# Kernel tuning notes

Hardware: AMD Instinct MI355X
Metric: run time of the kernel (lower is better)

Reference implementation:

```python
import jax, jax.numpy as jnp
import numpy as np

B, C, R = 1024, 256, 7          # batch, channels, ROI feature map res
PATCH, DIL = 16, 2              # correlation patch size, dilation_patch
REP = 1024                      # representation_size
FLAT = PATCH * PATCH * R * R    # 12544 = fc1 input dim


def setup_inputs() -> dict:
    key = jax.random.key(0)
    k = jax.random.split(key, 8)
    return {
        "patch1": jax.random.normal(k[0], (B, C, R, R), dtype=jnp.float32),
        "patch2": jax.random.normal(k[1], (B, C, R, R), dtype=jnp.float32),
        "W1": jax.random.normal(k[2], (REP, FLAT), dtype=jnp.float32) * 0.01,
        "b1": jnp.zeros((REP,), dtype=jnp.float32),
        "W2": jax.random.normal(k[3], (REP, REP), dtype=jnp.float32) * 0.02,
        "b2": jnp.zeros((REP,), dtype=jnp.float32),
        "W3": jax.random.normal(k[4], (4, REP), dtype=jnp.float32) * 0.02,
        "b3": jnp.zeros((4,), dtype=jnp.float32),
    }


def _correlate(p1, p2):
    """SpatialCorrelationSampler(patch_size=16, dilation_patch=2), kernel=1, stride=1.
    out[b, pi, pj, i, j] = sum_c p1[b,c,i,j] * p2[b,c, i+(pi-8)*2, j+(pj-8)*2]
    (zero outside bounds). Returns [B, PATCH*PATCH, R, R]."""
    pad = (PATCH // 2) * DIL  # 16; displacements span [-16, 14]
    p2p = jnp.pad(p2, ((0, 0), (0, 0), (pad, pad), (pad, pad)))  # [B,C,39,39]
    outs = []
    for pi in range(PATCH):
        for pj in range(PATCH):
            # shifted window: row offset (pi-8)*2 + pad = 2*pi, same for cols
            win = p2p[:, :, DIL * pi:DIL * pi + R, DIL * pj:DIL * pj + R]
            outs.append(jnp.einsum('bchw,bchw->bhw', p1, win))
    return jnp.stack(outs, axis=1)  # [B, 256, 7, 7] -> matches torch flatten order


def reference(patch1, patch2, W1, b1, W2, b2, W3, b3):
    x = _correlate(patch1, patch2).reshape(patch1.shape[0], -1)  # [B, 12544]
    x = jax.nn.relu(x @ W1.T + b1)
    x = jax.nn.relu(x @ W2.T + b2)
    pred_boxes = x @ W3.T + b3  # [B, 4]
    return pred_boxes
```

## Files before the change

kernel.cpp:

```cpp
#include <hip/hip_runtime.h>

#define BATCH 1024
#define RR    49
#define SP    12544
#define KVALID 625
#define KPAD   640
#define REP_N  1024

typedef __attribute__((ext_vector_type(4))) float f32x4;
typedef __attribute__((ext_vector_type(8))) short s16x8;

__device__ __forceinline__ unsigned short f2bf_rne(float f) {
    unsigned int u = __float_as_uint(f);
    unsigned int r = u + 0x7FFFu + ((u >> 16) & 1u);
    return (unsigned short)(r >> 16);
}
__device__ __forceinline__ float bf2f(unsigned short h) {
    return __uint_as_float(((unsigned int)h) << 16);
}
__device__ __forceinline__ void split2(float v, unsigned short& h, unsigned short& l) {
    h = f2bf_rne(v);
    l = f2bf_rne(v - bf2f(h));
}

__device__ __forceinline__ void dec25(int u, int& i, int& d) {
    int ii = (u >= 4) + (u >= 7) + (u >= 11) + (u >= 14) + (u >= 18) + (u >= 21);
    int cum = (7 * ii + 1) >> 1;
    i = ii;
    d = 2 * (u - cum) + (ii & 1);
}
__device__ __forceinline__ int enc25(int i, int d) {
    return ((7 * i + 1) >> 1) + ((d - (i & 1)) >> 1);
}

__device__ __forceinline__ int kflat_of(int a) {
    int ar = a / 25, ac = a % 25;
    int i, dy, j, dx;
    dec25(ar, i, dy);
    dec25(ac, j, dx);
    int pi = (dy + 16 - i) >> 1;
    int pj = (dx + 16 - j) >> 1;
    return (pi * 16 + pj) * 49 + i * 7 + j;
}

#define MM(d, a, b) d = __builtin_amdgcn_mfma_f32_16x16x32_bf16(a, b, d, 0, 0, 0)

__global__ __launch_bounds__(256) void corr_gram_kernel(
    const float* __restrict__ p1, const float* __restrict__ p2,
    unsigned short* __restrict__ xh, unsigned short* __restrict__ xl)
{
    __shared__ unsigned short Ah[64][72];
    __shared__ unsigned short Al[64][72];
    __shared__ unsigned short Bh[64][72];
    __shared__ unsigned short Bl[64][72];

    const int b = blockIdx.x;
    const int t = threadIdx.x;
    const float* P1 = p1 + (size_t)b * SP;
    const float* P2 = p2 + (size_t)b * SP;

    const int wv   = t >> 6;
    const int lane = t & 63;
    const int wr = (wv >> 1) * 32;
    const int wc = (wv & 1) * 32;
    const int fr = lane & 15;
    const int fg = (lane >> 4) * 8;

    f32x4 acc00 = {}, acc01 = {}, acc10 = {}, acc11 = {};

    for (int cc = 0; cc < 4; ++cc) {
        __syncthreads();
        for (int j = t; j < 784; j += 256) {
            const int isB = (j >= 392);
            const int jj = isB ? j - 392 : j;
            const float* P = isB ? P2 : P1;
            unsigned short* Hp = isB ? &Bh[0][0] : &Ah[0][0];
            unsigned short* Lp = isB ? &Bl[0][0] : &Al[0][0];
            const int cg = jj / 49;
            const int s  = jj - cg * 49;
            const float* src = P + (cc * 64 + cg * 8) * 49 + s;
            float v[8];
            #pragma unroll
            for (int i = 0; i < 8; ++i) v[i] = src[i * 49];
            s16x8 hv, lv;
            #pragma unroll
            for (int i = 0; i < 8; ++i) {
                unsigned short h, l;
                split2(v[i], h, l);
                hv[i] = (short)h; lv[i] = (short)l;
            }
            *(s16x8*)&Hp[s * 72 + cg * 8] = hv;
            *(s16x8*)&Lp[s * 72 + cg * 8] = lv;
        }
        __syncthreads();

        #pragma unroll
        for (int ks = 0; ks < 2; ++ks) {
            const int ko = ks * 32 + fg;
            s16x8 ah0 = *(const s16x8*)&Ah[wr + fr][ko];
            s16x8 ah1 = *(const s16x8*)&Ah[wr + 16 + fr][ko];
            s16x8 al0 = *(const s16x8*)&Al[wr + fr][ko];
            s16x8 al1 = *(const s16x8*)&Al[wr + 16 + fr][ko];
            s16x8 bh0 = *(const s16x8*)&Bh[wc + fr][ko];
            s16x8 bh1 = *(const s16x8*)&Bh[wc + 16 + fr][ko];
            s16x8 bl0 = *(const s16x8*)&Bl[wc + fr][ko];
            s16x8 bl1 = *(const s16x8*)&Bl[wc + 16 + fr][ko];

            MM(acc00, ah0, bh0); MM(acc00, ah0, bl0); MM(acc00, al0, bh0);
            MM(acc01, ah0, bh1); MM(acc01, ah0, bl1); MM(acc01, al0, bh1);
            MM(acc10, ah1, bh0); MM(acc10, ah1, bl0); MM(acc10, al1, bh0);
            MM(acc11, ah1, bh1); MM(acc11, ah1, bl1); MM(acc11, al1, bh1);
        }
    }

    if (t < KPAD - KVALID) {
        xh[(size_t)b * KPAD + KVALID + t] = 0;
        xl[(size_t)b * KPAD + KVALID + t] = 0;
    }

    unsigned short* rh = xh + (size_t)b * KPAD;
    unsigned short* rl = xl + (size_t)b * KPAD;
    const int arow = (lane >> 4) * 4;
    #pragma unroll
    for (int nf = 0; nf < 2; ++nf) {
        const int n = wc + nf * 16 + fr;
        #pragma unroll
        for (int mf = 0; mf < 2; ++mf) {
            const f32x4 a = (nf == 0) ? (mf == 0 ? acc00 : acc10)
                                      : (mf == 0 ? acc01 : acc11);
            #pragma unroll
            for (int r = 0; r < 4; ++r) {
                const int m = wr + mf * 16 + arow + r;
                if (m < RR && n < RR) {
                    const int i  = m / 7, jj = m - i * 7;
                    const int dy = n / 7, dx = n - dy * 7;
                    if ((((i + dy) | (jj + dx)) & 1) == 0) {
                        const int aidx = enc25(i, dy) * 25 + enc25(jj, dx);
                        unsigned short h, l;
                        split2(a[r], h, l);
                        rh[aidx] = h; rl[aidx] = l;
                    }
                }
            }
        }
    }
}

__global__ __launch_bounds__(256) void prep_w1_kernel(
    const float* __restrict__ W1,
    unsigned short* __restrict__ wh, unsigned short* __restrict__ wl)
{
    int idx = blockIdx.x * 256 + threadIdx.x;
    int n = idx / KPAD, a = idx - n * KPAD;
    float v = 0.f;
    if (a < KVALID) v = W1[(size_t)n * SP + kflat_of(a)];
    unsigned short h, l;
    split2(v, h, l);
    wh[idx] = h; wl[idx] = l;
}

__global__ __launch_bounds__(256) void prep_w2_kernel(
    const float* __restrict__ W2,
    unsigned short* __restrict__ wh, unsigned short* __restrict__ wl)
{
    int idx = (blockIdx.x * 256 + threadIdx.x) * 4;
    float4 v = *(const float4*)&W2[idx];
    unsigned short h0, l0, h1, l1, h2, l2, h3, l3;
    split2(v.x, h0, l0); split2(v.y, h1, l1);
    split2(v.z, h2, l2); split2(v.w, h3, l3);
    ushort4 hv = make_ushort4(h0, h1, h2, h3);
    ushort4 lv = make_ushort4(l0, l1, l2, l3);
    *(ushort4*)&wh[idx] = hv;
    *(ushort4*)&wl[idx] = lv;
}

template<bool SPLIT_OUT>
__global__ __launch_bounds__(256) void gemm_mfma(
    const unsigned short* __restrict__ Xh, const unsigned short* __restrict__ Xl, int ldx,
    const unsigned short* __restrict__ Wh, const unsigned short* __restrict__ Wl, int ldw,
    const float* __restrict__ bias, int K,
    float* __restrict__ Yf, unsigned short* __restrict__ Yh, unsigned short* __restrict__ Yl,
    int ldy)
{
    __shared__ unsigned short As[2][64][72];
    __shared__ unsigned short Bs[2][64][72];

    const int t = threadIdx.x;
    const int m_base = blockIdx.y * 64;
    const int n_base = blockIdx.x * 64;

    const int trow = t >> 2;
    const int tc   = (t & 3) * 8;

    const unsigned short* xh_p = Xh + (size_t)(m_base + trow) * ldx + tc;
    const unsigned short* xl_p = Xl + (size_t)(m_base + trow) * ldx + tc;
    const unsigned short* wh_p = Wh + (size_t)(n_base + trow) * ldw + tc;
    const unsigned short* wl_p = Wl + (size_t)(n_base + trow) * ldw + tc;

    const int wv   = t >> 6;
    const int lane = t & 63;
    const int wr = (wv >> 1) * 32;
    const int wc = (wv & 1) * 32;
    const int fr = lane & 15;
    const int fg = (lane >> 4) * 8;

    f32x4 acc00 = {}, acc01 = {}, acc10 = {}, acc11 = {};

    for (int k0 = 0; k0 < K; k0 += 64) {
        s16x8 vxh0 = *(const s16x8*)(xh_p + k0);
        s16x8 vxh1 = *(const s16x8*)(xh_p + k0 + 32);
        s16x8 vxl0 = *(const s16x8*)(xl_p + k0);
        s16x8 vxl1 = *(const s16x8*)(xl_p + k0 + 32);
        s16x8 vwh0 = *(const s16x8*)(wh_p + k0);
        s16x8 vwh1 = *(const s16x8*)(wh_p + k0 + 32);
        s16x8 vwl0 = *(const s16x8*)(wl_p + k0);
        s16x8 vwl1 = *(const s16x8*)(wl_p + k0 + 32);
        __syncthreads();
        *(s16x8*)&As[0][trow][tc]      = vxh0;
        *(s16x8*)&As[0][trow][tc + 32] = vxh1;
        *(s16x8*)&As[1][trow][tc]      = vxl0;
        *(s16x8*)&As[1][trow][tc + 32] = vxl1;
        *(s16x8*)&Bs[0][trow][tc]      = vwh0;
        *(s16x8*)&Bs[0][trow][tc + 32] = vwh1;
        *(s16x8*)&Bs[1][trow][tc]      = vwl0;
        *(s16x8*)&Bs[1][trow][tc + 32] = vwl1;
        __syncthreads();

        #pragma unroll
        for (int ks = 0; ks < 2; ++ks) {
            const int ko = ks * 32 + fg;
            s16x8 ah0 = *(const s16x8*)&As[0][wr + fr][ko];
            s16x8 ah1 = *(const s16x8*)&As[0][wr + 16 + fr][ko];
            s16x8 al0 = *(const s16x8*)&As[1][wr + fr][ko];
            s16x8 al1 = *(const s16x8*)&As[1][wr + 16 + fr][ko];
            s16x8 bh0 = *(const s16x8*)&Bs[0][wc + fr][ko];
            s16x8 bh1 = *(const s16x8*)&Bs[0][wc + 16 + fr][ko];
            s16x8 bl0 = *(const s16x8*)&Bs[1][wc + fr][ko];
            s16x8 bl1 = *(const s16x8*)&Bs[1][wc + 16 + fr][ko];

            MM(acc00, ah0, bh0); MM(acc00, ah0, bl0); MM(acc00, al0, bh0);
            MM(acc01, ah0, bh1); MM(acc01, ah0, bl1); MM(acc01, al0, bh1);
            MM(acc10, ah1, bh0); MM(acc10, ah1, bl0); MM(acc10, al1, bh0);
            MM(acc11, ah1, bh1); MM(acc11, ah1, bl1); MM(acc11, al1, bh1);
        }
    }

    const int arow = (lane >> 4) * 4;
    #pragma unroll
    for (int nf = 0; nf < 2; ++nf) {
        const int col = n_base + wc + nf * 16 + fr;
        const float bv = bias[col];
        #pragma unroll
        for (int mf = 0; mf < 2; ++mf) {
            const f32x4 a = (nf == 0) ? (mf == 0 ? acc00 : acc10)
                                      : (mf == 0 ? acc01 : acc11);
            #pragma unroll
            for (int r = 0; r < 4; ++r) {
                const int row = m_base + wr + mf * 16 + arow + r;
                float v = fmaxf(a[r] + bv, 0.f);
                if (SPLIT_OUT) {
                    unsigned short h, l;
                    split2(v, h, l);
                    Yh[(size_t)row * ldy + col] = h;
                    Yl[(size_t)row * ldy + col] = l;
                } else {
                    Yf[(size_t)row * ldy + col] = v;
                }
            }
        }
    }
}

__global__ __launch_bounds__(256) void head_kernel(
    const float* __restrict__ h2, const float* __restrict__ W3,
    const float* __restrict__ b3, float* __restrict__ out)
{
    const int b = blockIdx.x;
    const int t = threadIdx.x;
    const float* row = h2 + (size_t)b * REP_N;

    float a0 = 0.f, a1 = 0.f, a2 = 0.f, a3 = 0.f;
    for (int k = t; k < REP_N; k += 256) {
        float x = row[k];
        a0 = fmaf(x, W3[k],             a0);
        a1 = fmaf(x, W3[REP_N + k],     a1);
        a2 = fmaf(x, W3[2 * REP_N + k], a2);
        a3 = fmaf(x, W3[3 * REP_N + k], a3);
    }
    #pragma unroll
    for (int off = 32; off > 0; off >>= 1) {
        a0 += __shfl_down(a0, off);
        a1 += __shfl_down(a1, off);
        a2 += __shfl_down(a2, off);
        a3 += __shfl_down(a3, off);
    }
    __shared__ float red[4][4];
    int wid = t >> 6, lane = t & 63;
    if (lane == 0) { red[wid][0] = a0; red[wid][1] = a1; red[wid][2] = a2; red[wid][3] = a3; }
    __syncthreads();
    if (t < 4) {
        out[b * 4 + t] = red[0][t] + red[1][t] + red[2][t] + red[3][t] + b3[t];
    }
}

extern "C" void kernel_launch(void* const* d_in, const int* in_sizes, int n_in,
                              void* d_out, int out_size, void* d_ws, size_t ws_size,
                              hipStream_t stream) {
    const float* p1 = (const float*)d_in[0];
    const float* p2 = (const float*)d_in[1];
    const float* W1 = (const float*)d_in[2];
    const float* b1 = (const float*)d_in[3];
    const float* W2 = (const float*)d_in[4];
    const float* b2 = (const float*)d_in[5];
    const float* W3 = (const float*)d_in[6];
    const float* b3 = (const float*)d_in[7];
    float* out = (float*)d_out;

    char* ws = (char*)d_ws;
    unsigned short* xh  = (unsigned short*)(ws + 0);
    unsigned short* xl  = (unsigned short*)(ws + 1310720);
    unsigned short* w1h = (unsigned short*)(ws + 2621440);
    unsigned short* w1l = (unsigned short*)(ws + 3932160);
    float*          h2  = (float*)(ws + 0);
    unsigned short* h1h = (unsigned short*)(ws + 5242880);
    unsigned short* h1l = (unsigned short*)(ws + 7340032);
    unsigned short* w2h = (unsigned short*)(ws + 9437184);
    unsigned short* w2l = (unsigned short*)(ws + 11534336);

    corr_gram_kernel<<<BATCH, 256, 0, stream>>>(p1, p2, xh, xl);
    prep_w1_kernel<<<(REP_N * KPAD) / 256, 256, 0, stream>>>(W1, w1h, w1l);
    prep_w2_kernel<<<(REP_N * REP_N) / (256 * 4), 256, 0, stream>>>(W2, w2h, w2l);

    gemm_mfma<true><<<dim3(16, 16), 256, 0, stream>>>(
        xh, xl, KPAD, w1h, w1l, KPAD, b1, KPAD,
        (float*)nullptr, h1h, h1l, REP_N);

    gemm_mfma<false><<<dim3(16, 16), 256, 0, stream>>>(
        h1h, h1l, REP_N, w2h, w2l, REP_N, b2, REP_N,
        h2, (unsigned short*)nullptr, (unsigned short*)nullptr, REP_N);

    head_kernel<<<BATCH, 256, 0, stream>>>(h2, W3, b3, out);
}
```

Measured before the change: 68.23 us.

## Load correlation operands directly into registers and stage output in LDS

The gram kernel no longer stages p1/p2 through shared-memory tiles with barriers. Each lane now loads its MFMA operand fragments straight from global memory and splits them into bf16 hi/lo pairs with the packed v_cvt_pk_bf16_f32 instruction. The scattered per-element output writes are gathered into a small LDS buffer and then written out as coalesced 32-bit stores. The goal is to remove synchronization and LDS round-trips, at the cost of strided, redundant global loads across waves. Out-of-range rows are clamped to row 48, and the packed convert may round slightly differently than the manual RNE.

```diff
diff --git a/kernel.cpp b/kernel.cpp
--- a/kernel.cpp
+++ b/kernel.cpp
@@ -21,6 +21,24 @@
 __device__ __forceinline__ void split2(float v, unsigned short& h, unsigned short& l) {
     h = f2bf_rne(v);
     l = f2bf_rne(v - bf2f(h));
+}
+__device__ __forceinline__ unsigned int cvtpk_bf16(float a, float b) {
+    unsigned int r;
+    asm("v_cvt_pk_bf16_f32 %0, %1, %2" : "=v"(r) : "v"(a), "v"(b));
+    return r;
+}
+__device__ __forceinline__ void cvt8(const float* v, s16x8& hv, s16x8& lv) {
+    unsigned int* hp = (unsigned int*)&hv;
+    unsigned int* lp = (unsigned int*)&lv;
+    #pragma unroll
+    for (int i = 0; i < 4; ++i) {
+        float v0 = v[2 * i], v1 = v[2 * i + 1];
+        unsigned int ph = cvtpk_bf16(v0, v1);
+        float h0 = __uint_as_float(ph << 16);
+        float h1 = __uint_as_float(ph & 0xFFFF0000u);
+        unsigned int pl = cvtpk_bf16(v0 - h0, v1 - h1);
+        hp[i] = ph; lp[i] = pl;
+    }
 }
 
 __device__ __forceinline__ void dec25(int u, int& i, int& d) {
@@ -49,10 +67,8 @@
     const float* __restrict__ p1, const float* __restrict__ p2,
     unsigned short* __restrict__ xh, unsigned short* __restrict__ xl)
 {
-    __shared__ unsigned short Ah[64][72];
-    __shared__ unsigned short Al[64][72];
-    __shared__ unsigned short Bh[64][72];
-    __shared__ unsigned short Bl[64][72];
+    __shared__ unsigned short SXh[KPAD];
+    __shared__ unsigned short SXl[KPAD];
 
     const int b = blockIdx.x;
     const int t = threadIdx.x;
@@ -66,45 +82,38 @@
     const int fr = lane & 15;
     const int fg = (lane >> 4) * 8;
 
+    const int sa0 = wr + fr;
+    const int sa1 = min(wr + 16 + fr, 48);
+    const int sb0 = wc + fr;
+    const int sb1 = min(wc + 16 + fr, 48);
+
+    const float* pa0 = P1 + fg * 49 + sa0;
+    const float* pa1 = P1 + fg * 49 + sa1;
+    const float* pb0 = P2 + fg * 49 + sb0;
+    const float* pb1 = P2 + fg * 49 + sb1;
+
+    for (int i = t; i < KPAD; i += 256) { SXh[i] = 0; SXl[i] = 0; }
+
     f32x4 acc00 = {}, acc01 = {}, acc10 = {}, acc11 = {};
 
+    #pragma unroll
     for (int cc = 0; cc < 4; ++cc) {
-        __syncthreads();
-        for (int j = t; j < 784; j += 256) {
-            const int isB = (j >= 392);
-            const int jj = isB ? j - 392 : j;
-            const float* P = isB ? P2 : P1;
-            unsigned short* Hp = isB ? &Bh[0][0] : &Ah[0][0];
-            unsigned short* Lp = isB ? &Bl[0][0] : &Al[0][0];
-            const int cg = jj / 49;
-            const int s  = jj - cg * 49;
-            const float* src = P + (cc * 64 + cg * 8) * 49 + s;
-            float v[8];
-            #pragma unroll
-            for (int i = 0; i < 8; ++i) v[i] = src[i * 49];
-            s16x8 hv, lv;
+        #pragma unroll
+        for (int ks = 0; ks < 2; ++ks) {
+            const int co = (cc * 64 + ks * 32) * 49;
+            float a0f[8], a1f[8], b0f[8], b1f[8];
             #pragma unroll
             for (int i = 0; i < 8; ++i) {
-                unsigned short h, l;
-                split2(v[i], h, l);
-                hv[i] = (short)h; lv[i] = (short)l;
+                a0f[i] = pa0[co + i * 49];
+                a1f[i] = pa1[co + i * 49];
+                b0f[i] = pb0[co + i * 49];
+                b1f[i] = pb1[co + i * 49];
             }
-            *(s16x8*)&Hp[s * 72 + cg * 8] = hv;
-            *(s16x8*)&Lp[s * 72 + cg * 8] = lv;
-        }
-        __syncthreads();
-
-        #pragma unroll
-        for (int ks = 0; ks < 2; ++ks) {
-            const int ko = ks * 32 + fg;
-            s16x8 ah0 = *(const s16x8*)&Ah[wr + fr][ko];
-            s16x8 ah1 = *(const s16x8*)&Ah[wr + 16 + fr][ko];
-            s16x8 al0 = *(const s16x8*)&Al[wr + fr][ko];
-            s16x8 al1 = *(const s16x8*)&Al[wr + 16 + fr][ko];
-            s16x8 bh0 = *(const s16x8*)&Bh[wc + fr][ko];
-            s16x8 bh1 = *(const s16x8*)&Bh[wc + 16 + fr][ko];
-            s16x8 bl0 = *(const s16x8*)&Bl[wc + fr][ko];
-            s16x8 bl1 = *(const s16x8*)&Bl[wc + 16 + fr][ko];
+            s16x8 ah0, al0, ah1, al1, bh0, bl0, bh1, bl1;
+            cvt8(a0f, ah0, al0);
+            cvt8(a1f, ah1, al1);
+            cvt8(b0f, bh0, bl0);
+            cvt8(b1f, bh1, bl1);
 
             MM(acc00, ah0, bh0); MM(acc00, ah0, bl0); MM(acc00, al0, bh0);
             MM(acc01, ah0, bh1); MM(acc01, ah0, bl1); MM(acc01, al0, bh1);
@@ -113,13 +122,6 @@
         }
     }
 
-    if (t < KPAD - KVALID) {
-        xh[(size_t)b * KPAD + KVALID + t] = 0;
-        xl[(size_t)b * KPAD + KVALID + t] = 0;
-    }
-
-    unsigned short* rh = xh + (size_t)b * KPAD;
-    unsigned short* rl = xl + (size_t)b * KPAD;
     const int arow = (lane >> 4) * 4;
     #pragma unroll
     for (int nf = 0; nf < 2; ++nf) {
@@ -138,12 +140,19 @@
                         const int aidx = enc25(i, dy) * 25 + enc25(jj, dx);
                         unsigned short h, l;
                         split2(a[r], h, l);
-                        rh[aidx] = h; rl[aidx] = l;
+                        SXh[aidx] = h; SXl[aidx] = l;
                     }
                 }
             }
         }
     }
+    __syncthreads();
+
+    unsigned int* rh = (unsigned int*)(xh + (size_t)b * KPAD);
+    unsigned int* rl = (unsigned int*)(xl + (size_t)b * KPAD);
+    const unsigned int* sh = (const unsigned int*)SXh;
+    const unsigned int* sl = (const unsigned int*)SXl;
+    for (int i = t; i < KPAD / 2; i += 256) { rh[i] = sh[i]; rl[i] = sl[i]; }
 }
 
 __global__ __launch_bounds__(256) void prep_w1_kernel(
```

Measured after the change: 66.72 us. 1.02x faster.
